# Optimization experiments

Measured on AMD Instinct MI355X. Metric: run time of the kernel, lower is better.

The kernel has to match this reference:

```python
import jax, jax.numpy as jnp
import numpy as np

D_MODEL = 1024
NHEAD = 16
D_HEAD = D_MODEL // NHEAD


def setup_inputs() -> dict:
    key = jax.random.key(0)
    ks = jax.random.split(key, 9)
    B, S = 2, 2048
    scale = 1.0 / np.sqrt(D_MODEL)
    x = jax.random.normal(ks[0], (B, S, D_MODEL), dtype=jnp.float32)
    Wq = jax.random.normal(ks[1], (D_MODEL, D_MODEL), dtype=jnp.float32) * scale
    Wk = jax.random.normal(ks[2], (D_MODEL, D_MODEL), dtype=jnp.float32) * scale
    Wv = jax.random.normal(ks[3], (D_MODEL, D_MODEL), dtype=jnp.float32) * scale
    Wo = jax.random.normal(ks[4], (D_MODEL, D_MODEL), dtype=jnp.float32) * scale
    bq = jax.random.normal(ks[5], (D_MODEL,), dtype=jnp.float32) * 0.01
    bk = jax.random.normal(ks[6], (D_MODEL,), dtype=jnp.float32) * 0.01
    bv = jax.random.normal(ks[7], (D_MODEL,), dtype=jnp.float32) * 0.01
    bo = jax.random.normal(ks[8], (D_MODEL,), dtype=jnp.float32) * 0.01
    return {"x": x, "Wq": Wq, "bq": bq, "Wk": Wk, "bk": bk,
            "Wv": Wv, "bv": bv, "Wo": Wo, "bo": bo}


def reference(x, Wq, bq, Wk, bk, Wv, bv, Wo, bo):
    B, S, D = x.shape
    H, Dh = NHEAD, D_HEAD
    # projections; weights stored as (in, out) so y = x @ W + b
    def split_heads(t):  # [B,S,D] -> [B,H,S,Dh]
        return t.reshape(B, S, H, Dh).transpose(0, 2, 1, 3)
    q = split_heads(x @ Wq + bq)
    k = split_heads(x @ Wk + bk)
    v = split_heads(x @ Wv + bv)
    scale = 1.0 / jnp.sqrt(jnp.asarray(Dh, dtype=x.dtype))
    attn = jnp.einsum("bhqd,bhkd->bhqk", q, k) * scale  # [B,H,S,S]
    attn = jax.nn.softmax(attn, axis=-1)
    out = jnp.einsum("bhqk,bhkd->bhqd", attn, v)  # [B,H,S,Dh]
    out = out.transpose(0, 2, 1, 3).reshape(B, S, D)
    return out @ Wo + bo
```

## Files before the change

kernel.cpp:

```cpp
#include <hip/hip_runtime.h>
#include <hip/hip_bf16.h>
#include <stdint.h>
#include <stddef.h>

typedef __bf16 b16;
typedef __bf16 b16x4 __attribute__((ext_vector_type(4)));
typedef __bf16 b16x8 __attribute__((ext_vector_type(8)));
typedef float  f32x4 __attribute__((ext_vector_type(4)));

#define LOG2E 1.4426950408889634f
#define QSCALE (0.125f * LOG2E)

#if __has_builtin(__builtin_amdgcn_exp2f)
#define EXP2F(x) __builtin_amdgcn_exp2f(x)
#else
#define EXP2F(x) exp2f(x)
#endif

typedef __attribute__((address_space(1))) void gvoid;
typedef __attribute__((address_space(3))) void svoid;

__device__ __forceinline__ void async_cp16(void* lds, const void* g) {
    __builtin_amdgcn_global_load_lds((gvoid*)(void*)g, (svoid*)lds, 16, 0, 0);
}

__global__ __launch_bounds__(256) void k_cvt_x(const float* __restrict__ x,
                                               b16* __restrict__ xb) {
    int i = (blockIdx.x * 256 + threadIdx.x) * 4;
    float4 v = *(const float4*)(x + i);
    b16x4 o = { (b16)v.x, (b16)v.y, (b16)v.z, (b16)v.w };
    *(b16x4*)(xb + i) = o;
}

__global__ __launch_bounds__(256) void k_transpose(const float* __restrict__ Wq,
                                                   const float* __restrict__ Wk,
                                                   const float* __restrict__ Wv,
                                                   const float* __restrict__ Wo,
                                                   b16* __restrict__ WtQKV,
                                                   b16* __restrict__ Wot) {
    __shared__ float t[32][33];
    const int z = blockIdx.z;
    const float* W = (z == 0) ? Wq : (z == 1) ? Wk : (z == 2) ? Wv : Wo;
    const int k0 = blockIdx.x * 32, n0 = blockIdx.y * 32;
    const int tr = threadIdx.x >> 3, tc4 = (threadIdx.x & 7) * 4;
    float4 v = *(const float4*)(W + (size_t)(k0 + tr) * 1024 + n0 + tc4);
    t[tr][tc4 + 0] = v.x; t[tr][tc4 + 1] = v.y;
    t[tr][tc4 + 2] = v.z; t[tr][tc4 + 3] = v.w;
    __syncthreads();
    b16* dst = (z < 3) ? (WtQKV + ((size_t)z << 20)) : Wot;
    b16x4 o = { (b16)t[tc4 + 0][tr], (b16)t[tc4 + 1][tr],
                (b16)t[tc4 + 2][tr], (b16)t[tc4 + 3][tr] };
    *(b16x4*)(dst + (size_t)(n0 + tr) * 1024 + k0 + tc4) = o;
}

__device__ __forceinline__ void gemm128_core(const b16* __restrict__ Ab,
                                             const b16* __restrict__ Bb,
                                             b16* As, b16* Bs, int tid,
                                             f32x4 acc[4][4]) {
    const int lane = tid & 63, wave = tid >> 6;
    const int wm = wave & 1, wn = wave >> 1;
    const int quad = lane >> 4, lc = lane & 15;
    const int ci0 = tid, ci1 = tid + 256;
    for (int k0 = 0; k0 < 1024; k0 += 32) {
        __syncthreads();
        async_cp16(As + ci0 * 8, Ab + (ci0 >> 2) * 1024 + k0 + (ci0 & 3) * 8);
        async_cp16(As + ci1 * 8, Ab + (ci1 >> 2) * 1024 + k0 + (ci1 & 3) * 8);
        async_cp16(Bs + ci0 * 8, Bb + (ci0 >> 2) * 1024 + k0 + (ci0 & 3) * 8);
        async_cp16(Bs + ci1 * 8, Bb + (ci1 >> 2) * 1024 + k0 + (ci1 & 3) * 8);
        __syncthreads();
        b16x8 af[4], bfr[4];
#pragma unroll
        for (int mt = 0; mt < 4; ++mt)
            af[mt] = *(const b16x8*)(As + (wm * 64 + mt * 16 + lc) * 32 + quad * 8);
#pragma unroll
        for (int nt = 0; nt < 4; ++nt)
            bfr[nt] = *(const b16x8*)(Bs + (wn * 64 + nt * 16 + lc) * 32 + quad * 8);
#pragma unroll
        for (int mt = 0; mt < 4; ++mt)
#pragma unroll
            for (int nt = 0; nt < 4; ++nt)
                acc[mt][nt] = __builtin_amdgcn_mfma_f32_16x16x32_bf16(
                    af[mt], bfr[nt], acc[mt][nt], 0, 0, 0);
    }
}

__global__ __launch_bounds__(256, 2) void k_gemm_qkv(
    const b16* __restrict__ A, const b16* __restrict__ Bt,
    const float* __restrict__ bq, const float* __restrict__ bk,
    const float* __restrict__ bv,
    b16* __restrict__ Qg, b16* __restrict__ Kg, b16* __restrict__ Vtg) {
    __shared__ __align__(16) b16 As[128 * 32];
    __shared__ __align__(16) b16 Bs[128 * 32];
    const int bm = blockIdx.x, bn = blockIdx.y;
    const int tid = threadIdx.x;
    const int lane = tid & 63, wave = tid >> 6;
    const int wm = wave & 1, wn = wave >> 1;
    const int quad = lane >> 4, lc = lane & 15;

    f32x4 acc[4][4] = {};
    gemm128_core(A + (size_t)(bm * 128) * 1024, Bt + (size_t)(bn * 128) * 1024,
                 As, Bs, tid, acc);

    const int mat = bn >> 3;
    const float* bp = (mat == 0) ? bq : (mat == 1) ? bk : bv;
#pragma unroll
    for (int nt = 0; nt < 4; ++nt) {
        const int n = bn * 128 + wn * 64 + nt * 16 + lc;
        const int cm = n & 1023;
        const int h = cm >> 6, dh = cm & 63;
        const float bval = bp[cm];
#pragma unroll
        for (int mt = 0; mt < 4; ++mt) {
            const int m0 = bm * 128 + wm * 64 + mt * 16 + quad * 4;
            const int b = m0 >> 11;
            const int bh = b * 16 + h;
            const int s0 = m0 & 2047;
            if (mat == 2) {
                b16x4 o;
#pragma unroll
                for (int r = 0; r < 4; ++r) o[r] = (b16)(acc[mt][nt][r] + bval);
                *(b16x4*)(Vtg + (size_t)(bh * 64 + dh) * 2048 + s0) = o;
            } else if (mat == 0) {
#pragma unroll
                for (int r = 0; r < 4; ++r)
                    Qg[(size_t)(bh * 2048 + s0 + r) * 64 + dh] =
                        (b16)((acc[mt][nt][r] + bval) * QSCALE);
            } else {
#pragma unroll
                for (int r = 0; r < 4; ++r)
                    Kg[(size_t)(bh * 2048 + s0 + r) * 64 + dh] =
                        (b16)(acc[mt][nt][r] + bval);
            }
        }
    }
}

__global__ __launch_bounds__(256, 2) void k_flash(
    const b16* __restrict__ Qg, const b16* __restrict__ Kg,
    const b16* __restrict__ Vtg,
    float* __restrict__ Opart, float* __restrict__ lpart,
    b16* __restrict__ AO, int ktiles, int direct) {
    __shared__ __align__(16) b16 Ks[64 * 64];
    __shared__ __align__(16) b16 Vs[64 * 64];
    __shared__ __align__(16) b16 Ps[256 * 72];
    const int qb = blockIdx.x;
    const int bh = blockIdx.y;
    const int part = blockIdx.z;
    const int tid = threadIdx.x, lane = tid & 63, wave = tid >> 6;
    const int quad = lane >> 4, lc = lane & 15;

    const b16* Qbase = Qg + ((size_t)bh * 2048 + qb * 256 + wave * 64) * 64;
    b16x8 qf[4][2];
#pragma unroll
    for (int qt = 0; qt < 4; ++qt)
#pragma unroll
        for (int ch = 0; ch < 2; ++ch)
            qf[qt][ch] = *(const b16x8*)(Qbase + (qt * 16 + lc) * 64 + ch * 32 + quad * 8);

    f32x4 oacc[4][4] = {};
    float lsum[4] = {0.f, 0.f, 0.f, 0.f};

    const b16* Kbh = Kg + (size_t)bh * 2048 * 64;
    const b16* Vbh = Vtg + (size_t)bh * 64 * 2048;
    b16* Pw = Ps + wave * (64 * 72);
    const int kt0 = part * ktiles;

    for (int kt = kt0; kt < kt0 + ktiles; ++kt) {
        __syncthreads();
#pragma unroll
        for (int i = 0; i < 2; ++i) {
            const int ci = tid + i * 256;
            const int r = ci >> 3, cs = ci & 7;
            const int gc = cs ^ (r & 7);
            async_cp16(Ks + ci * 8, Kbh + (size_t)(kt * 64 + r) * 64 + gc * 8);
            async_cp16(Vs + ci * 8, Vbh + (size_t)r * 2048 + kt * 64 + gc * 8);
        }
        __syncthreads();

#pragma unroll
        for (int m = 0; m < 4; ++m) {
            b16x8 kf[2];
#pragma unroll
            for (int ch = 0; ch < 2; ++ch) {
                const int row = m * 16 + lc;
                const int chunk = (ch * 4 + quad) ^ (row & 7);
                kf[ch] = *(const b16x8*)(Ks + row * 64 + chunk * 8);
            }
#pragma unroll
            for (int qt = 0; qt < 4; ++qt) {
                f32x4 s = {};
                s = __builtin_amdgcn_mfma_f32_16x16x32_bf16(kf[0], qf[qt][0], s, 0, 0, 0);
                s = __builtin_amdgcn_mfma_f32_16x16x32_bf16(kf[1], qf[qt][1], s, 0, 0, 0);
                float e0 = EXP2F(s[0]), e1 = EXP2F(s[1]);
                float e2 = EXP2F(s[2]), e3 = EXP2F(s[3]);
                lsum[qt] += (e0 + e1) + (e2 + e3);
                b16x4 p = { (b16)e0, (b16)e1, (b16)e2, (b16)e3 };
                *(b16x4*)(Pw + (qt * 16 + lc) * 72 + m * 16 + quad * 4) = p;
            }
        }

#pragma unroll
        for (int ks = 0; ks < 2; ++ks) {
            b16x8 vf[4], pf[4];
#pragma unroll
            for (int dt = 0; dt < 4; ++dt) {
                const int row = dt * 16 + lc;
                const int chunk = (ks * 4 + quad) ^ (row & 7);
                vf[dt] = *(const b16x8*)(Vs + row * 64 + chunk * 8);
            }
#pragma unroll
            for (int mt = 0; mt < 4; ++mt)
                pf[mt] = *(const b16x8*)(Pw + (mt * 16 + lc) * 72 + ks * 32 + quad * 8);
#pragma unroll
            for (int mt = 0; mt < 4; ++mt)
#pragma unroll
                for (int dt = 0; dt < 4; ++dt)
                    oacc[mt][dt] = __builtin_amdgcn_mfma_f32_16x16x32_bf16(
                        pf[mt], vf[dt], oacc[mt][dt], 0, 0, 0);
        }
    }

#pragma unroll
    for (int qt = 0; qt < 4; ++qt) {
        lsum[qt] += __shfl_xor(lsum[qt], 16, 64);
        lsum[qt] += __shfl_xor(lsum[qt], 32, 64);
    }

    if (!direct) {
        float* Op = Opart + ((size_t)(part * 32 + bh) * 2048 + qb * 256 + wave * 64) * 64;
#pragma unroll
        for (int mt = 0; mt < 4; ++mt)
#pragma unroll
            for (int dt = 0; dt < 4; ++dt)
#pragma unroll
                for (int r = 0; r < 4; ++r)
                    Op[(mt * 16 + quad * 4 + r) * 64 + dt * 16 + lc] = oacc[mt][dt][r];
        if (quad == 0) {
            float* lp = lpart + (size_t)(part * 32 + bh) * 2048 + qb * 256 + wave * 64;
#pragma unroll
            for (int qt = 0; qt < 4; ++qt) lp[qt * 16 + lc] = lsum[qt];
        }
    } else {
        float* Ls = (float*)(void*)Pw;
        if (quad == 0) {
#pragma unroll
            for (int qt = 0; qt < 4; ++qt) Ls[qt * 16 + lc] = lsum[qt];
        }
        const int b = bh >> 4, h = bh & 15;
#pragma unroll
        for (int mt = 0; mt < 4; ++mt)
#pragma unroll
            for (int r = 0; r < 4; ++r) {
                const float inv = 1.0f / Ls[mt * 16 + quad * 4 + r];
                const int s = qb * 256 + wave * 64 + mt * 16 + quad * 4 + r;
#pragma unroll
                for (int dt = 0; dt < 4; ++dt)
                    AO[(size_t)(b * 2048 + s) * 1024 + h * 64 + dt * 16 + lc] =
                        (b16)(oacc[mt][dt][r] * inv);
            }
    }
}

__global__ __launch_bounds__(256) void k_merge(const float* __restrict__ Opart,
                                               const float* __restrict__ lpart,
                                               b16* __restrict__ AO, int np) {
    const int bh = blockIdx.y;
    const int q = blockIdx.x * 16 + (threadIdx.x >> 4);
    const int d4 = (threadIdx.x & 15) * 4;
    const size_t qi = (size_t)bh * 2048 + q;
    f32x4 o = *(const f32x4*)(Opart + qi * 64 + d4);
    float l = lpart[qi];
    if (np == 2) {
        o += *(const f32x4*)(Opart + (qi + (size_t)32 * 2048) * 64 + d4);
        l += lpart[qi + (size_t)32 * 2048];
    }
    const float inv = 1.0f / l;
    const int b = bh >> 4, h = bh & 15;
    b16x4 ob = { (b16)(o[0] * inv), (b16)(o[1] * inv),
                 (b16)(o[2] * inv), (b16)(o[3] * inv) };
    *(b16x4*)(AO + (size_t)(b * 2048 + q) * 1024 + h * 64 + d4) = ob;
}

__global__ __launch_bounds__(256, 2) void k_gemm_out(
    const b16* __restrict__ A, const b16* __restrict__ Bt,
    const float* __restrict__ bo, float* __restrict__ out) {
    __shared__ __align__(16) b16 As[128 * 32];
    __shared__ __align__(16) b16 Bs[128 * 32];
    const int bm = blockIdx.x, bn = blockIdx.y;
    const int tid = threadIdx.x;
    const int lane = tid & 63, wave = tid >> 6;
    const int wm = wave & 1, wn = wave >> 1;
    const int quad = lane >> 4, lc = lane & 15;

    f32x4 acc[4][4] = {};
    gemm128_core(A + (size_t)(bm * 128) * 1024, Bt + (size_t)(bn * 128) * 1024,
                 As, Bs, tid, acc);

#pragma unroll
    for (int nt = 0; nt < 4; ++nt) {
        const int n = bn * 128 + wn * 64 + nt * 16 + lc;
        const float bval = bo[n];
#pragma unroll
        for (int mt = 0; mt < 4; ++mt) {
            const int m0 = bm * 128 + wm * 64 + mt * 16 + quad * 4;
#pragma unroll
            for (int r = 0; r < 4; ++r)
                out[(size_t)(m0 + r) * 1024 + n] = acc[mt][nt][r] + bval;
        }
    }
}

extern "C" void kernel_launch(void* const* d_in, const int* in_sizes, int n_in,
                              void* d_out, int out_size, void* d_ws, size_t ws_size,
                              hipStream_t stream) {
    const float* x  = (const float*)d_in[0];
    const float* Wq = (const float*)d_in[1];
    const float* bq = (const float*)d_in[2];
    const float* Wk = (const float*)d_in[3];
    const float* bk = (const float*)d_in[4];
    const float* Wv = (const float*)d_in[5];
    const float* bv = (const float*)d_in[6];
    const float* Wo = (const float*)d_in[7];
    const float* bo = (const float*)d_in[8];
    float* out = (float*)d_out;

    char* ws = (char*)d_ws;
    const size_t MB = 1024 * 1024;
    b16* Xb  = (b16*)(ws);
    b16* AO  = (b16*)(ws);
    b16* WtQ = (b16*)(ws + 8 * MB);
    b16* Wot = (b16*)(ws + 14 * MB);
    b16* Qg  = (b16*)(ws + 16 * MB);
    b16* Kg  = (b16*)(ws + 24 * MB);
    b16* Vtg = (b16*)(ws + 32 * MB);

    const size_t need2 = 40 * MB + 2 * (16 * MB) + 2 * 256 * 1024;
    const int np = (ws_size >= need2) ? 2 : 1;
    float* Opart = (float*)(ws + 40 * MB);
    float* lpart = (float*)(ws + 40 * MB + (size_t)np * 16 * MB);
    const int direct = (np == 1);

    k_cvt_x<<<4096, 256, 0, stream>>>(x, Xb);
    k_transpose<<<dim3(32, 32, 4), 256, 0, stream>>>(Wq, Wk, Wv, Wo, WtQ, Wot);
    k_gemm_qkv<<<dim3(32, 24), 256, 0, stream>>>(Xb, WtQ, bq, bk, bv, Qg, Kg, Vtg);
    k_flash<<<dim3(8, 32, np), 256, 0, stream>>>(Qg, Kg, Vtg, Opart, lpart, AO,
                                                 32 / np, direct);
    if (!direct)
        k_merge<<<dim3(128, 32), 256, 0, stream>>>(Opart, lpart, AO, np);
    k_gemm_out<<<dim3(32, 8), 256, 0, stream>>>(AO, Wot, bo, out);
}
```

Before: 201.0 us.

## Double-buffer LDS in GEMMs and flash, shrink P buffer, split keys four ways

New measurement: 296.0 us. 1.47x slower.

```diff
diff --git a/kernel.cpp b/kernel.cpp
--- a/kernel.cpp
+++ b/kernel.cpp
@@ -53,6 +53,18 @@
     *(b16x4*)(dst + (size_t)(n0 + tr) * 1024 + k0 + tc4) = o;
 }
 
+__device__ __forceinline__ void gemm_stage(const b16* __restrict__ Ab,
+                                           const b16* __restrict__ Bb,
+                                           b16* As, b16* Bs, int buf, int k0, int tid) {
+    const int ci0 = tid, ci1 = tid + 256;
+    b16* Ad = As + buf * 4096;
+    b16* Bd = Bs + buf * 4096;
+    async_cp16(Ad + ci0 * 8, Ab + (size_t)(ci0 >> 2) * 1024 + k0 + (ci0 & 3) * 8);
+    async_cp16(Ad + ci1 * 8, Ab + (size_t)(ci1 >> 2) * 1024 + k0 + (ci1 & 3) * 8);
+    async_cp16(Bd + ci0 * 8, Bb + (size_t)(ci0 >> 2) * 1024 + k0 + (ci0 & 3) * 8);
+    async_cp16(Bd + ci1 * 8, Bb + (size_t)(ci1 >> 2) * 1024 + k0 + (ci1 & 3) * 8);
+}
+
 __device__ __forceinline__ void gemm128_core(const b16* __restrict__ Ab,
                                              const b16* __restrict__ Bb,
                                              b16* As, b16* Bs, int tid,
@@ -60,37 +72,38 @@
     const int lane = tid & 63, wave = tid >> 6;
     const int wm = wave & 1, wn = wave >> 1;
     const int quad = lane >> 4, lc = lane & 15;
-    const int ci0 = tid, ci1 = tid + 256;
+    gemm_stage(Ab, Bb, As, Bs, 0, 0, tid);
+    int cur = 0;
     for (int k0 = 0; k0 < 1024; k0 += 32) {
         __syncthreads();
-        async_cp16(As + ci0 * 8, Ab + (ci0 >> 2) * 1024 + k0 + (ci0 & 3) * 8);
-        async_cp16(As + ci1 * 8, Ab + (ci1 >> 2) * 1024 + k0 + (ci1 & 3) * 8);
-        async_cp16(Bs + ci0 * 8, Bb + (ci0 >> 2) * 1024 + k0 + (ci0 & 3) * 8);
-        async_cp16(Bs + ci1 * 8, Bb + (ci1 >> 2) * 1024 + k0 + (ci1 & 3) * 8);
-        __syncthreads();
+        const int kn = (k0 + 32 < 1024) ? k0 + 32 : 0;
+        gemm_stage(Ab, Bb, As, Bs, cur ^ 1, kn, tid);
+        const b16* Ac = As + cur * 4096;
+        const b16* Bc = Bs + cur * 4096;
         b16x8 af[4], bfr[4];
 #pragma unroll
         for (int mt = 0; mt < 4; ++mt)
-            af[mt] = *(const b16x8*)(As + (wm * 64 + mt * 16 + lc) * 32 + quad * 8);
+            af[mt] = *(const b16x8*)(Ac + (wm * 64 + mt * 16 + lc) * 32 + quad * 8);
 #pragma unroll
         for (int nt = 0; nt < 4; ++nt)
-            bfr[nt] = *(const b16x8*)(Bs + (wn * 64 + nt * 16 + lc) * 32 + quad * 8);
+            bfr[nt] = *(const b16x8*)(Bc + (wn * 64 + nt * 16 + lc) * 32 + quad * 8);
 #pragma unroll
         for (int mt = 0; mt < 4; ++mt)
 #pragma unroll
             for (int nt = 0; nt < 4; ++nt)
                 acc[mt][nt] = __builtin_amdgcn_mfma_f32_16x16x32_bf16(
                     af[mt], bfr[nt], acc[mt][nt], 0, 0, 0);
-    }
-}
-
-__global__ __launch_bounds__(256, 2) void k_gemm_qkv(
+        cur ^= 1;
+    }
+}
+
+__global__ __launch_bounds__(256, 3) void k_gemm_qkv(
     const b16* __restrict__ A, const b16* __restrict__ Bt,
     const float* __restrict__ bq, const float* __restrict__ bk,
     const float* __restrict__ bv,
     b16* __restrict__ Qg, b16* __restrict__ Kg, b16* __restrict__ Vtg) {
-    __shared__ __align__(16) b16 As[128 * 32];
-    __shared__ __align__(16) b16 Bs[128 * 32];
+    __shared__ __align__(16) b16 As[2 * 128 * 32];
+    __shared__ __align__(16) b16 Bs[2 * 128 * 32];
     const int bm = blockIdx.x, bn = blockIdx.y;
     const int tid = threadIdx.x;
     const int lane = tid & 63, wave = tid >> 6;
@@ -135,14 +148,14 @@
     }
 }
 
-__global__ __launch_bounds__(256, 2) void k_flash(
+__global__ __launch_bounds__(256, 3) void k_flash(
     const b16* __restrict__ Qg, const b16* __restrict__ Kg,
     const b16* __restrict__ Vtg,
     float* __restrict__ Opart, float* __restrict__ lpart,
     b16* __restrict__ AO, int ktiles, int direct) {
-    __shared__ __align__(16) b16 Ks[64 * 64];
-    __shared__ __align__(16) b16 Vs[64 * 64];
-    __shared__ __align__(16) b16 Ps[256 * 72];
+    __shared__ __align__(16) b16 Ks[2][64 * 64];
+    __shared__ __align__(16) b16 Vs[2][64 * 64];
+    __shared__ __align__(16) b16 Ps[4][64 * 40];
     const int qb = blockIdx.x;
     const int bh = blockIdx.y;
     const int part = blockIdx.z;
@@ -162,55 +175,60 @@
 
     const b16* Kbh = Kg + (size_t)bh * 2048 * 64;
     const b16* Vbh = Vtg + (size_t)bh * 64 * 2048;
-    b16* Pw = Ps + wave * (64 * 72);
-    const int kt0 = part * ktiles;
-
-    for (int kt = kt0; kt < kt0 + ktiles; ++kt) {
+    b16* Pw = Ps[wave];
+    const int kt0 = part * ktiles, ktend = kt0 + ktiles;
+
+    const int ciA = tid, ciB = tid + 256;
+    const int rA = ciA >> 3, gA = (ciA & 7) ^ (rA & 7);
+    const int rB = ciB >> 3, gB = (ciB & 7) ^ (rB & 7);
+
+    {
+        async_cp16(&Ks[0][ciA * 8], Kbh + (size_t)(kt0 * 64 + rA) * 64 + gA * 8);
+        async_cp16(&Ks[0][ciB * 8], Kbh + (size_t)(kt0 * 64 + rB) * 64 + gB * 8);
+        async_cp16(&Vs[0][ciA * 8], Vbh + (size_t)rA * 2048 + kt0 * 64 + gA * 8);
+        async_cp16(&Vs[0][ciB * 8], Vbh + (size_t)rB * 2048 + kt0 * 64 + gB * 8);
+    }
+    int cur = 0;
+
+    for (int kt = kt0; kt < ktend; ++kt) {
         __syncthreads();
-#pragma unroll
-        for (int i = 0; i < 2; ++i) {
-            const int ci = tid + i * 256;
-            const int r = ci >> 3, cs = ci & 7;
-            const int gc = cs ^ (r & 7);
-            async_cp16(Ks + ci * 8, Kbh + (size_t)(kt * 64 + r) * 64 + gc * 8);
-            async_cp16(Vs + ci * 8, Vbh + (size_t)r * 2048 + kt * 64 + gc * 8);
-        }
-        __syncthreads();
-
-#pragma unroll
-        for (int m = 0; m < 4; ++m) {
-            b16x8 kf[2];
-#pragma unroll
-            for (int ch = 0; ch < 2; ++ch) {
-                const int row = m * 16 + lc;
-                const int chunk = (ch * 4 + quad) ^ (row & 7);
-                kf[ch] = *(const b16x8*)(Ks + row * 64 + chunk * 8);
+        const int nk = (kt + 1 < ktend) ? kt + 1 : kt0;
+        const int nb = cur ^ 1;
+        async_cp16(&Ks[nb][ciA * 8], Kbh + (size_t)(nk * 64 + rA) * 64 + gA * 8);
+        async_cp16(&Ks[nb][ciB * 8], Kbh + (size_t)(nk * 64 + rB) * 64 + gB * 8);
+        async_cp16(&Vs[nb][ciA * 8], Vbh + (size_t)rA * 2048 + nk * 64 + gA * 8);
+        async_cp16(&Vs[nb][ciB * 8], Vbh + (size_t)rB * 2048 + nk * 64 + gB * 8);
+
+        const b16* Kc = Ks[cur];
+        const b16* Vc = Vs[cur];
+#pragma unroll
+        for (int half = 0; half < 2; ++half) {
+#pragma unroll
+            for (int m2 = 0; m2 < 2; ++m2) {
+                const int row = (half * 2 + m2) * 16 + lc;
+                const b16x8 kf0 = *(const b16x8*)(Kc + row * 64 + ((quad) ^ (row & 7)) * 8);
+                const b16x8 kf1 = *(const b16x8*)(Kc + row * 64 + ((4 + quad) ^ (row & 7)) * 8);
+#pragma unroll
+                for (int qt = 0; qt < 4; ++qt) {
+                    f32x4 s = {};
+                    s = __builtin_amdgcn_mfma_f32_16x16x32_bf16(kf0, qf[qt][0], s, 0, 0, 0);
+                    s = __builtin_amdgcn_mfma_f32_16x16x32_bf16(kf1, qf[qt][1], s, 0, 0, 0);
+                    const float e0 = EXP2F(s[0]), e1 = EXP2F(s[1]);
+                    const float e2 = EXP2F(s[2]), e3 = EXP2F(s[3]);
+                    lsum[qt] += (e0 + e1) + (e2 + e3);
+                    b16x4 p = { (b16)e0, (b16)e1, (b16)e2, (b16)e3 };
+                    *(b16x4*)(Pw + (qt * 16 + lc) * 40 + m2 * 16 + quad * 4) = p;
+                }
             }
-#pragma unroll
-            for (int qt = 0; qt < 4; ++qt) {
-                f32x4 s = {};
-                s = __builtin_amdgcn_mfma_f32_16x16x32_bf16(kf[0], qf[qt][0], s, 0, 0, 0);
-                s = __builtin_amdgcn_mfma_f32_16x16x32_bf16(kf[1], qf[qt][1], s, 0, 0, 0);
-                float e0 = EXP2F(s[0]), e1 = EXP2F(s[1]);
-                float e2 = EXP2F(s[2]), e3 = EXP2F(s[3]);
-                lsum[qt] += (e0 + e1) + (e2 + e3);
-                b16x4 p = { (b16)e0, (b16)e1, (b16)e2, (b16)e3 };
-                *(b16x4*)(Pw + (qt * 16 + lc) * 72 + m * 16 + quad * 4) = p;
-            }
-        }
-
-#pragma unroll
-        for (int ks = 0; ks < 2; ++ks) {
             b16x8 vf[4], pf[4];
 #pragma unroll
             for (int dt = 0; dt < 4; ++dt) {
                 const int row = dt * 16 + lc;
-                const int chunk = (ks * 4 + quad) ^ (row & 7);
-                vf[dt] = *(const b16x8*)(Vs + row * 64 + chunk * 8);
+                vf[dt] = *(const b16x8*)(Vc + row * 64 + ((half * 4 + quad) ^ (row & 7)) * 8);
             }
 #pragma unroll
             for (int mt = 0; mt < 4; ++mt)
-                pf[mt] = *(const b16x8*)(Pw + (mt * 16 + lc) * 72 + ks * 32 + quad * 8);
+                pf[mt] = *(const b16x8*)(Pw + (mt * 16 + lc) * 40 + quad * 8);
 #pragma unroll
             for (int mt = 0; mt < 4; ++mt)
 #pragma unroll
@@ -218,6 +236,7 @@
                     oacc[mt][dt] = __builtin_amdgcn_mfma_f32_16x16x32_bf16(
                         pf[mt], vf[dt], oacc[mt][dt], 0, 0, 0);
         }
+        cur ^= 1;
     }
 
 #pragma unroll
@@ -270,9 +289,9 @@
     const size_t qi = (size_t)bh * 2048 + q;
     f32x4 o = *(const f32x4*)(Opart + qi * 64 + d4);
     float l = lpart[qi];
-    if (np == 2) {
-        o += *(const f32x4*)(Opart + (qi + (size_t)32 * 2048) * 64 + d4);
-        l += lpart[qi + (size_t)32 * 2048];
+    for (int p = 1; p < np; ++p) {
+        o += *(const f32x4*)(Opart + (qi + (size_t)p * 32 * 2048) * 64 + d4);
+        l += lpart[qi + (size_t)p * 32 * 2048];
     }
     const float inv = 1.0f / l;
     const int b = bh >> 4, h = bh & 15;
@@ -284,25 +303,55 @@
 __global__ __launch_bounds__(256, 2) void k_gemm_out(
     const b16* __restrict__ A, const b16* __restrict__ Bt,
     const float* __restrict__ bo, float* __restrict__ out) {
-    __shared__ __align__(16) b16 As[128 * 32];
-    __shared__ __align__(16) b16 Bs[128 * 32];
+    __shared__ __align__(16) b16 As[2 * 64 * 32];
+    __shared__ __align__(16) b16 Bs[2 * 128 * 32];
     const int bm = blockIdx.x, bn = blockIdx.y;
     const int tid = threadIdx.x;
     const int lane = tid & 63, wave = tid >> 6;
     const int wm = wave & 1, wn = wave >> 1;
     const int quad = lane >> 4, lc = lane & 15;
-
-    f32x4 acc[4][4] = {};
-    gemm128_core(A + (size_t)(bm * 128) * 1024, Bt + (size_t)(bn * 128) * 1024,
-                 As, Bs, tid, acc);
+    const b16* Ab = A + (size_t)(bm * 64) * 1024;
+    const b16* Bb = Bt + (size_t)(bn * 128) * 1024;
+
+    const int ci0 = tid, ci1 = tid + 256;
+    async_cp16(&As[ci0 * 8], Ab + (size_t)(ci0 >> 2) * 1024 + (ci0 & 3) * 8);
+    async_cp16(&Bs[ci0 * 8], Bb + (size_t)(ci0 >> 2) * 1024 + (ci0 & 3) * 8);
+    async_cp16(&Bs[ci1 * 8], Bb + (size_t)(ci1 >> 2) * 1024 + (ci1 & 3) * 8);
+
+    f32x4 acc[2][4] = {};
+    int cur = 0;
+    for (int k0 = 0; k0 < 1024; k0 += 32) {
+        __syncthreads();
+        const int kn = (k0 + 32 < 1024) ? k0 + 32 : 0;
+        const int nb = cur ^ 1;
+        async_cp16(&As[nb * 2048 + ci0 * 8], Ab + (size_t)(ci0 >> 2) * 1024 + kn + (ci0 & 3) * 8);
+        async_cp16(&Bs[nb * 4096 + ci0 * 8], Bb + (size_t)(ci0 >> 2) * 1024 + kn + (ci0 & 3) * 8);
+        async_cp16(&Bs[nb * 4096 + ci1 * 8], Bb + (size_t)(ci1 >> 2) * 1024 + kn + (ci1 & 3) * 8);
+        const b16* Ac = &As[cur * 2048];
+        const b16* Bc = &Bs[cur * 4096];
+        b16x8 af[2], bfr[4];
+#pragma unroll
+        for (int mt = 0; mt < 2; ++mt)
+            af[mt] = *(const b16x8*)(Ac + (wm * 32 + mt * 16 + lc) * 32 + quad * 8);
+#pragma unroll
+        for (int nt = 0; nt < 4; ++nt)
+            bfr[nt] = *(const b16x8*)(Bc + (wn * 64 + nt * 16 + lc) * 32 + quad * 8);
+#pragma unroll
+        for (int mt = 0; mt < 2; ++mt)
+#pragma unroll
+            for (int nt = 0; nt < 4; ++nt)
+                acc[mt][nt] = __builtin_amdgcn_mfma_f32_16x16x32_bf16(
+                    af[mt], bfr[nt], acc[mt][nt], 0, 0, 0);
+        cur ^= 1;
+    }
 
 #pragma unroll
     for (int nt = 0; nt < 4; ++nt) {
         const int n = bn * 128 + wn * 64 + nt * 16 + lc;
         const float bval = bo[n];
 #pragma unroll
-        for (int mt = 0; mt < 4; ++mt) {
-            const int m0 = bm * 128 + wm * 64 + mt * 16 + quad * 4;
+        for (int mt = 0; mt < 2; ++mt) {
+            const int m0 = bm * 64 + wm * 32 + mt * 16 + quad * 4;
 #pragma unroll
             for (int r = 0; r < 4; ++r)
                 out[(size_t)(m0 + r) * 1024 + n] = acc[mt][nt][r] + bval;
@@ -334,10 +383,12 @@
     b16* Kg  = (b16*)(ws + 24 * MB);
     b16* Vtg = (b16*)(ws + 32 * MB);
 
-    const size_t need2 = 40 * MB + 2 * (16 * MB) + 2 * 256 * 1024;
-    const int np = (ws_size >= need2) ? 2 : 1;
-    float* Opart = (float*)(ws + 40 * MB);
-    float* lpart = (float*)(ws + 40 * MB + (size_t)np * 16 * MB);
+    const size_t base = 40 * MB;
+    int np = 1;
+    if (ws_size >= base + 4 * 16 * MB + 4 * 256 * 1024) np = 4;
+    else if (ws_size >= base + 2 * 16 * MB + 2 * 256 * 1024) np = 2;
+    float* Opart = (float*)(ws + base);
+    float* lpart = (float*)(ws + base + (size_t)np * 16 * MB);
     const int direct = (np == 1);
 
     k_cvt_x<<<4096, 256, 0, stream>>>(x, Xb);
@@ -347,5 +398,5 @@
                                                  32 / np, direct);
     if (!direct)
         k_merge<<<dim3(128, 32), 256, 0, stream>>>(Opart, lpart, AO, np);
-    k_gemm_out<<<dim3(32, 8), 256, 0, stream>>>(AO, Wot, bo, out);
-}
+    k_gemm_out<<<dim3(64, 8), 256, 0, stream>>>(AO, Wot, bo, out);
+}
```
